# Performance work log

Measured on AMD Instinct MI355X. Metric: run time of the kernel, lower is better.

Reference implementation:

```python
import jax, jax.numpy as jnp
import numpy as np

N_NODES = 100000


def _gcn_conv(x, edge_index, W, b):
    """PyG GCNConv: add self-loops, symmetric deg^-1/2 normalization, scatter-add."""
    N = x.shape[0]
    h = x @ W  # [N, out]
    src = edge_index[0]
    dst = edge_index[1]
    loop = jnp.arange(N, dtype=src.dtype)
    src = jnp.concatenate([src, loop])
    dst = jnp.concatenate([dst, loop])
    deg = jax.ops.segment_sum(jnp.ones(src.shape[0], dtype=h.dtype), dst, num_segments=N)
    dinv = jnp.where(deg > 0, jax.lax.rsqrt(deg), 0.0)
    norm = dinv[src] * dinv[dst]  # [E+N]
    msgs = h[src] * norm[:, None]  # gather + scale
    out = jax.ops.segment_sum(msgs, dst, num_segments=N)  # scatter-add
    return out + b


def setup_inputs() -> dict:
    key = jax.random.key(0)
    k1, k2, k3, k4 = jax.random.split(key, 4)
    F_IN, H = 512, 16
    x = jax.random.normal(k1, (N_NODES, F_IN), dtype=jnp.float32)
    edge_index = jax.random.randint(k2, (2, 3200000), 0, N_NODES, dtype=jnp.int64)
    # Glorot init like PyG GCNConv
    lim = np.sqrt(6.0 / (F_IN + H)).astype(np.float32)
    W1 = jax.random.uniform(k3, (F_IN, H), dtype=jnp.float32, minval=-lim, maxval=lim)
    b1 = jnp.zeros((H,), dtype=jnp.float32)
    return {"x": x, "edge_index": edge_index, "W1": W1, "b1": b1}


def reference(x, edge_index, W1, b1):
    # forward: relu(GCNConv(x)); dropout is identity in eval; log_softmax over features
    h = jax.nn.relu(_gcn_conv(x, edge_index, W1, b1))
    return jax.nn.log_softmax(h, axis=1)
```

## Files before the change

### kernel.cpp

```cpp
#include <hip/hip_runtime.h>
#include <hip/hip_bf16.h>
#include <stdint.h>

#define N_NODES 100000
#define F_IN    512
#define HOUT    16

#define BSH   8
#define NBUK  391
#define CAP   9216
#define CHUNK 4096
#define GEMM_BLOCKS 782

typedef __attribute__((ext_vector_type(8))) short bf16x8;
typedef __attribute__((ext_vector_type(4))) float f32x4;

__device__ __forceinline__ short f2bf(float f) {
    union { float f; uint32_t u; } v; v.f = f;
    uint32_t r = (v.u + 0x7FFFu + ((v.u >> 16) & 1u)) >> 16;
    return (short)r;
}
__device__ __forceinline__ float bf2f(uint32_t bits16) {
    union { uint32_t u; float f; } v; v.u = bits16 << 16;
    return v.f;
}

__device__ __forceinline__ int edge_at(const void* ei, int64_t idx, uint32_t is64) {
    if (is64) return (int)((const long long*)ei)[idx];
    return ((const int*)ei)[idx];
}

__global__ void k_init(const uint32_t* __restrict__ e_u32, uint32_t* __restrict__ flag,
                       uint32_t* __restrict__ bucket_woff) {
    const int t = threadIdx.x;
    if (t < NBUK) bucket_woff[t] = 0u;
    if (t == 0) {
        uint32_t o = 0;
        #pragma unroll
        for (int i = 1; i < 32; i += 2) o |= e_u32[i];
        flag[0] = (o == 0u) ? 1u : 0u;
    }
}

__global__ __launch_bounds__(512) void k_fused(const void* __restrict__ ei, int E, int nchunks,
                                               const uint32_t* __restrict__ flag,
                                               uint32_t* __restrict__ bucket_woff,
                                               uint32_t* __restrict__ gpairs,
                                               const float* __restrict__ x,
                                               const float* __restrict__ W,
                                               ushort* __restrict__ hb) {
    __shared__ uint32_t h[512];
    __shared__ uint32_t ex[512];
    __shared__ uint32_t pcnt[512];
    __shared__ uint32_t gbase[512];
    __shared__ uint32_t sorted[CHUNK];
    __shared__ uint16_t sbuck[CHUNK];

    const int t = threadIdx.x;

    if ((int)blockIdx.x < nchunks) {
        const uint32_t is64 = flag[0];
        const int base = blockIdx.x * CHUNK;
        const int chunk_n = min(CHUNK, E - base);
        const bool evenE = ((E & 1) == 0);

        h[t] = 0;
        __syncthreads();

        uint32_t pr[8];
        uint16_t bk[8];
        #pragma unroll
        for (int k = 0; k < 4; ++k) {
            const int e0 = base + k * 1024 + 2 * t;
            uint32_t s0 = 0, s1 = 0, d0 = 0, d1 = 0;
            const bool ok0 = (e0 < E), ok1 = (e0 + 1 < E);
            if (ok1 && evenE) {
                if (is64) {
                    ulonglong2 S = *(const ulonglong2*)((const long long*)ei + e0);
                    ulonglong2 D = *(const ulonglong2*)((const long long*)ei + (int64_t)E + e0);
                    s0 = (uint32_t)S.x; s1 = (uint32_t)S.y;
                    d0 = (uint32_t)D.x; d1 = (uint32_t)D.y;
                } else {
                    uint2 S = *(const uint2*)((const int*)ei + e0);
                    uint2 D = *(const uint2*)((const int*)ei + (int64_t)E + e0);
                    s0 = S.x; s1 = S.y; d0 = D.x; d1 = D.y;
                }
            } else {
                if (ok0) { s0 = (uint32_t)edge_at(ei, e0, is64);
                           d0 = (uint32_t)edge_at(ei, (int64_t)E + e0, is64); }
                if (ok1) { s1 = (uint32_t)edge_at(ei, e0 + 1, is64);
                           d1 = (uint32_t)edge_at(ei, (int64_t)E + e0 + 1, is64); }
            }
            bk[2*k]   = 0xFFFFu;
            bk[2*k+1] = 0xFFFFu;
            if (ok0) {
                uint32_t b = d0 >> BSH;
                pr[2*k] = (s0 << BSH) | (d0 & 255u);
                bk[2*k] = (uint16_t)b;
                atomicAdd(&h[b], 1u);
            }
            if (ok1) {
                uint32_t b = d1 >> BSH;
                pr[2*k+1] = (s1 << BSH) | (d1 & 255u);
                bk[2*k+1] = (uint16_t)b;
                atomicAdd(&h[b], 1u);
            }
        }
        __syncthreads();

        const uint32_t hv = h[t];
        uint32_t v = hv;
        #pragma unroll
        for (int d = 1; d < 64; d <<= 1) {
            uint32_t u = __shfl_up(v, d, 64);
            if ((t & 63) >= d) v += u;
        }
        h[t] = v;
        __syncthreads();
        uint32_t wbase = 0;
        const int w = t >> 6;
        for (int w2 = 0; w2 < w; ++w2) wbase += h[w2 * 64 + 63];
        const uint32_t exv = wbase + v - hv;
        ex[t] = exv;
        pcnt[t] = exv;
        if (t < NBUK) gbase[t] = atomicAdd(&bucket_woff[t], hv);
        __syncthreads();

        #pragma unroll
        for (int k = 0; k < 8; ++k) {
            if (bk[k] != 0xFFFFu) {
                uint32_t slot = atomicAdd(&pcnt[bk[k]], 1u);
                sorted[slot] = pr[k];
                sbuck[slot] = bk[k];
            }
        }
        __syncthreads();

        #pragma unroll
        for (int k = 0; k < 8; ++k) {
            int i = k * 512 + t;
            if (i < chunk_n) {
                uint32_t b = sbuck[i];
                uint32_t pos = gbase[b] + ((uint32_t)i - ex[b]);
                gpairs[(size_t)b * CAP + pos] = sorted[i];
            }
        }
    } else {
        const int lane = t & 63;
        const int wid  = t >> 6;
        const int tile = ((int)blockIdx.x - nchunks) * 8 + wid;
        if (tile * 16 >= N_NODES) return;
        const int c    = lane & 15;
        const int half = lane >> 4;

        bf16x8 bfrag[16];
        #pragma unroll
        for (int s = 0; s < 16; ++s) {
            #pragma unroll
            for (int e = 0; e < 8; ++e) {
                int k = 32 * s + 8 * half + e;
                bfrag[s][e] = f2bf(W[k * HOUT + c]);
            }
        }

        const int row = tile * 16 + c;
        const float* xr = x + (int64_t)row * F_IN;
        f32x4 acc = {0.f, 0.f, 0.f, 0.f};
        #pragma unroll
        for (int s = 0; s < 16; ++s) {
            const float4 a0 = *(const float4*)(xr + 32 * s + 8 * half);
            const float4 a1 = *(const float4*)(xr + 32 * s + 8 * half + 4);
            bf16x8 af;
            af[0] = f2bf(a0.x); af[1] = f2bf(a0.y); af[2] = f2bf(a0.z); af[3] = f2bf(a0.w);
            af[4] = f2bf(a1.x); af[5] = f2bf(a1.y); af[6] = f2bf(a1.z); af[7] = f2bf(a1.w);
            acc = __builtin_amdgcn_mfma_f32_16x16x32_bf16(af, bfrag[s], acc, 0, 0, 0);
        }

        #pragma unroll
        for (int r = 0; r < 4; ++r) {
            int orow = tile * 16 + 4 * half + r;
            hb[(int64_t)orow * HOUT + c] = (ushort)f2bf(acc[r]);
        }
    }
}

__global__ __launch_bounds__(256) void k_hist(const uint32_t* __restrict__ bucket_woff,
                                              const uint32_t* __restrict__ gpairs,
                                              uint32_t* __restrict__ cnt,
                                              ushort* __restrict__ hb) {
    const int b = blockIdx.x;
    const int t = threadIdx.x;
    const uint32_t count = bucket_woff[b];
    const uint32_t* gp = gpairs + (size_t)b * CAP;

    __shared__ uint32_t lc[256];
    lc[t] = 0;
    __syncthreads();
    for (uint32_t i = t; i < count; i += 256)
        atomicAdd(&lc[gp[i] & 255u], 1u);
    __syncthreads();

    const int gn = (b << BSH) + t;
    if (gn < N_NODES) {
        const uint32_t deg = lc[t];
        cnt[gn] = deg;
        const float dinv = rsqrtf((float)(deg + 1u));
        ushort* row = hb + (size_t)gn * HOUT;
        ulonglong4 rv = *(const ulonglong4*)row;
        ushort u[16];
        *(ulonglong4*)u = rv;
        #pragma unroll
        for (int q = 0; q < 16; ++q)
            u[q] = (ushort)f2bf(bf2f(u[q]) * dinv);
        *(ulonglong4*)row = *(const ulonglong4*)u;
    }
}

__global__ __launch_bounds__(1024) void k_sortagg(const uint32_t* __restrict__ bucket_woff,
                                                  const uint32_t* __restrict__ gpairs,
                                                  const uint32_t* __restrict__ cnt,
                                                  const ushort* __restrict__ hb,
                                                  const float* __restrict__ bias,
                                                  float* __restrict__ out) {
    const int bk = blockIdx.x;
    const int t = threadIdx.x;
    const uint32_t count = bucket_woff[bk];
    const uint32_t* gp = gpairs + (size_t)bk * CAP;
    const uint32_t* hb32 = (const uint32_t*)hb;

    __shared__ uint32_t lc[256];
    __shared__ uint32_t st[256];
    __shared__ uint32_t cur[256];
    __shared__ uint32_t lsrc[CAP];

    if (t < 256) {
        int gn = (bk << BSH) + t;
        lc[t] = (gn < N_NODES) ? cnt[gn] : 0u;
    }
    __syncthreads();
    if (t < 256) {
        const uint32_t hv = lc[t];
        uint32_t v = hv;
        #pragma unroll
        for (int d = 1; d < 64; d <<= 1) {
            uint32_t u = __shfl_up(v, d, 64);
            if ((t & 63) >= d) v += u;
        }
        cur[t] = v;
    }
    __syncthreads();
    if (t < 256) {
        uint32_t wb = 0;
        const int w = t >> 6;
        for (int w2 = 0; w2 < w; ++w2) wb += cur[w2 * 64 + 63];
        const uint32_t s = wb + cur[t] - lc[t];
        st[t] = s;
    }
    __syncthreads();
    if (t < 256) cur[t] = st[t];
    __syncthreads();

    for (uint32_t i = t; i < count; i += 1024) {
        uint32_t p = gp[i];
        uint32_t pos = atomicAdd(&cur[p & 255u], 1u);
        lsrc[pos] = p >> BSH;
    }
    __syncthreads();

    const int f8 = t & 7;
    const int g  = t >> 3;
    const float b0 = bias[2 * f8];
    const float b1 = bias[2 * f8 + 1];

    #pragma unroll
    for (int i = 0; i < 2; ++i) {
        int dl = g + 128 * i;
        int gn = (bk << BSH) + dl;
        if (gn >= N_NODES) break;
        const uint32_t s0 = st[dl];
        const uint32_t n  = lc[dl];

        float a0 = 0.f, a1 = 0.f;
        uint32_t j = 0;
        for (; j + 4 <= n; j += 4) {
            uint32_t sA = lsrc[s0 + j],     sB = lsrc[s0 + j + 1];
            uint32_t sC = lsrc[s0 + j + 2], sD = lsrc[s0 + j + 3];
            uint32_t uA = hb32[(size_t)sA * 8 + f8];
            uint32_t uB = hb32[(size_t)sB * 8 + f8];
            uint32_t uC = hb32[(size_t)sC * 8 + f8];
            uint32_t uD = hb32[(size_t)sD * 8 + f8];
            a0 += (bf2f(uA & 0xFFFFu) + bf2f(uB & 0xFFFFu))
                + (bf2f(uC & 0xFFFFu) + bf2f(uD & 0xFFFFu));
            a1 += (bf2f(uA >> 16) + bf2f(uB >> 16))
                + (bf2f(uC >> 16) + bf2f(uD >> 16));
        }
        for (; j < n; ++j) {
            uint32_t u = hb32[(size_t)lsrc[s0 + j] * 8 + f8];
            a0 += bf2f(u & 0xFFFFu);
            a1 += bf2f(u >> 16);
        }

        const float dinv = rsqrtf((float)(n + 1u));
        const uint32_t us = hb32[(size_t)gn * 8 + f8];
        float v0 = fmaxf(fmaf(dinv, a0 + bf2f(us & 0xFFFFu), b0), 0.f);
        float v1 = fmaxf(fmaf(dinv, a1 + bf2f(us >> 16), b1), 0.f);

        float m = fmaxf(v0, v1);
        #pragma unroll
        for (int d = 1; d < 8; d <<= 1) m = fmaxf(m, __shfl_xor(m, d, 8));
        float sum = __expf(v0 - m) + __expf(v1 - m);
        #pragma unroll
        for (int d = 1; d < 8; d <<= 1) sum += __shfl_xor(sum, d, 8);
        const float ls = m + __logf(sum);

        float2 o; o.x = v0 - ls; o.y = v1 - ls;
        ((float2*)out)[(size_t)gn * 8 + f8] = o;
    }
}

extern "C" void kernel_launch(void* const* d_in, const int* in_sizes, int n_in,
                              void* d_out, int out_size, void* d_ws, size_t ws_size,
                              hipStream_t stream) {
    const float* x  = (const float*)d_in[0];
    const void*  ei = d_in[1];
    const float* W  = (const float*)d_in[2];
    const float* b  = (const float*)d_in[3];
    float* out = (float*)d_out;
    const int E = in_sizes[1] / 2;
    const int nchunks = (E + CHUNK - 1) / CHUNK;

    char* ws = (char*)d_ws;
    uint32_t* flag        = (uint32_t*)ws;
    uint32_t* bucket_woff = (uint32_t*)(ws + 1024);
    uint32_t* gpairs      = (uint32_t*)(ws + (1 << 20));
    ushort*   hb          = (ushort*)(ws + (16 << 20));
    uint32_t* cnt         = (uint32_t*)(ws + (20 << 20));

    k_init<<<1, 512, 0, stream>>>((const uint32_t*)ei, flag, bucket_woff);
    k_fused<<<nchunks + GEMM_BLOCKS, 512, 0, stream>>>(ei, E, nchunks, flag,
                                                       bucket_woff, gpairs, x, W, hb);
    k_hist<<<NBUK, 256, 0, stream>>>(bucket_woff, gpairs, cnt, hb);
    k_sortagg<<<NBUK, 1024, 0, stream>>>(bucket_woff, gpairs, cnt, hb, b, out);
}
```

Measured before the change: 108.3 us.

## Stage bf16 W fragments in LDS and software-pipeline x loads in GEMM branch

The GEMM branch of the fused kernel now converts W to bf16 once per block into shared memory that aliases the sort buffers, instead of each lane holding 16 bf16x8 fragments in registers. The x row loads are software-pipelined with a 3-deep rotating register buffer so global loads run ahead of the MFMA. launch_bounds adds a minimum of 4 blocks per CU to cap register use. The aim is lower VGPR pressure, higher occupancy and better latency hiding, at the cost of an extra __syncthreads and LDS reads per MFMA step.

```diff
diff --git a/kernel.cpp b/kernel.cpp
--- a/kernel.cpp
+++ b/kernel.cpp
@@ -42,23 +42,24 @@
     }
 }
 
-__global__ __launch_bounds__(512) void k_fused(const void* __restrict__ ei, int E, int nchunks,
-                                               const uint32_t* __restrict__ flag,
-                                               uint32_t* __restrict__ bucket_woff,
-                                               uint32_t* __restrict__ gpairs,
-                                               const float* __restrict__ x,
-                                               const float* __restrict__ W,
-                                               ushort* __restrict__ hb) {
+__global__ __launch_bounds__(512, 4) void k_fused(const void* __restrict__ ei, int E, int nchunks,
+                                                  const uint32_t* __restrict__ flag,
+                                                  uint32_t* __restrict__ bucket_woff,
+                                                  uint32_t* __restrict__ gpairs,
+                                                  const float* __restrict__ x,
+                                                  const float* __restrict__ W,
+                                                  ushort* __restrict__ hb) {
     __shared__ uint32_t h[512];
     __shared__ uint32_t ex[512];
     __shared__ uint32_t pcnt[512];
     __shared__ uint32_t gbase[512];
-    __shared__ uint32_t sorted[CHUNK];
-    __shared__ uint16_t sbuck[CHUNK];
+    __shared__ __align__(16) uint32_t big[CHUNK + CHUNK / 2];
 
     const int t = threadIdx.x;
 
     if ((int)blockIdx.x < nchunks) {
+        uint32_t* sorted = big;
+        uint16_t* sbuck  = (uint16_t*)(big + CHUNK);
         const uint32_t is64 = flag[0];
         const int base = blockIdx.x * CHUNK;
         const int chunk_n = min(CHUNK, E - base);
@@ -146,6 +147,21 @@
             }
         }
     } else {
+        ushort* wlds = (ushort*)big;
+        #pragma unroll
+        for (int r = 0; r < 2; ++r) {
+            const int ent = t + 512 * r;
+            const int s  = ent >> 6;
+            const int hf = (ent >> 4) & 3;
+            const int c  = ent & 15;
+            ushort u[8];
+            #pragma unroll
+            for (int e = 0; e < 8; ++e)
+                u[e] = (ushort)f2bf(W[(32 * s + 8 * hf + e) * HOUT + c]);
+            *(ulonglong2*)(wlds + (size_t)ent * 8) = *(const ulonglong2*)u;
+        }
+        __syncthreads();
+
         const int lane = t & 63;
         const int wid  = t >> 6;
         const int tile = ((int)blockIdx.x - nchunks) * 8 + wid;
@@ -153,27 +169,32 @@
         const int c    = lane & 15;
         const int half = lane >> 4;
 
-        bf16x8 bfrag[16];
+        const int row = tile * 16 + c;
+        const float* xr = x + (int64_t)row * F_IN + half * 8;
+        const ushort* wb = wlds + (size_t)(half * 16 + c) * 8;
+
+        float4 xa[3], xb[3];
+        #pragma unroll
+        for (int p = 0; p < 3; ++p) {
+            xa[p] = *(const float4*)(xr + 32 * p);
+            xb[p] = *(const float4*)(xr + 32 * p + 4);
+        }
+
+        f32x4 acc = {0.f, 0.f, 0.f, 0.f};
         #pragma unroll
         for (int s = 0; s < 16; ++s) {
-            #pragma unroll
-            for (int e = 0; e < 8; ++e) {
-                int k = 32 * s + 8 * half + e;
-                bfrag[s][e] = f2bf(W[k * HOUT + c]);
-            }
-        }
-
-        const int row = tile * 16 + c;
-        const float* xr = x + (int64_t)row * F_IN;
-        f32x4 acc = {0.f, 0.f, 0.f, 0.f};
-        #pragma unroll
-        for (int s = 0; s < 16; ++s) {
-            const float4 a0 = *(const float4*)(xr + 32 * s + 8 * half);
-            const float4 a1 = *(const float4*)(xr + 32 * s + 8 * half + 4);
+            const int p = s % 3;
+            bf16x8 bf = *(const bf16x8*)(wb + (size_t)s * 512);
             bf16x8 af;
-            af[0] = f2bf(a0.x); af[1] = f2bf(a0.y); af[2] = f2bf(a0.z); af[3] = f2bf(a0.w);
-            af[4] = f2bf(a1.x); af[5] = f2bf(a1.y); af[6] = f2bf(a1.z); af[7] = f2bf(a1.w);
-            acc = __builtin_amdgcn_mfma_f32_16x16x32_bf16(af, bfrag[s], acc, 0, 0, 0);
+            af[0] = f2bf(xa[p].x); af[1] = f2bf(xa[p].y);
+            af[2] = f2bf(xa[p].z); af[3] = f2bf(xa[p].w);
+            af[4] = f2bf(xb[p].x); af[5] = f2bf(xb[p].y);
+            af[6] = f2bf(xb[p].z); af[7] = f2bf(xb[p].w);
+            if (s + 3 < 16) {
+                xa[p] = *(const float4*)(xr + 32 * (s + 3));
+                xb[p] = *(const float4*)(xr + 32 * (s + 3) + 4);
+            }
+            acc = __builtin_amdgcn_mfma_f32_16x16x32_bf16(af, bf, acc, 0, 0, 0);
         }
 
         #pragma unroll
@@ -253,8 +274,7 @@
         uint32_t wb = 0;
         const int w = t >> 6;
         for (int w2 = 0; w2 < w; ++w2) wb += cur[w2 * 64 + 63];
-        const uint32_t s = wb + cur[t] - lc[t];
-        st[t] = s;
+        st[t] = wb + cur[t] - lc[t];
     }
     __syncthreads();
     if (t < 256) cur[t] = st[t];
```

Measured after the change: 107.2 us. No clear change (-1.0%).
